# Kernel tuning notes

Hardware: AMD Instinct MI355X
Metric: run time of the kernel (lower is better)

Reference implementation:

```python
import jax, jax.numpy as jnp
import numpy as np

TIME_LEN = 8
JOINT_NUM = 22
SEQ = TIME_LEN * JOINT_NUM  # 176
H_NUM = 8
H_DIM = 64
NEG = -9e15


def build_t_mask():
    # ones everywhere, zero the 22x22 diagonal (same-frame) blocks, then add identity
    t = np.ones((SEQ, SEQ), dtype=np.float32)
    for i in range(TIME_LEN):
        b = i * JOINT_NUM
        t[b:b + JOINT_NUM, b:b + JOINT_NUM] = 0.0
    t += np.eye(SEQ, dtype=np.float32)
    return jnp.asarray(t)


def setup_inputs() -> dict:
    key = jax.random.key(0)
    ks = jax.random.split(key, 7)
    B, S, D_IN = 512, SEQ, 128
    D_MODEL = H_NUM * H_DIM
    s = 1.0 / np.sqrt(D_IN)
    return {
        "x": jax.random.normal(ks[0], (B, S, D_IN), dtype=jnp.float32),
        "Wq": jax.random.normal(ks[1], (D_IN, D_MODEL), dtype=jnp.float32) * s,
        "bq": jax.random.normal(ks[2], (D_MODEL,), dtype=jnp.float32) * 0.01,
        "Wk": jax.random.normal(ks[3], (D_IN, D_MODEL), dtype=jnp.float32) * s,
        "bk": jax.random.normal(ks[4], (D_MODEL,), dtype=jnp.float32) * 0.01,
        "Wv": jax.random.normal(ks[5], (D_IN, D_MODEL), dtype=jnp.float32) * s,
        "bv": jax.random.normal(ks[6], (D_MODEL,), dtype=jnp.float32) * 0.01,
    }


def reference(x, Wq, bq, Wk, bk, Wv, bv):
    B = x.shape[0]
    mask = build_t_mask()  # [S, S], values in {0, 1}
    # projections; dropout is inference-mode identity; value path has ReLU
    q = (x @ Wq + bq).reshape(B, -1, H_NUM, H_DIM).transpose(0, 2, 1, 3)  # [B,H,S,D]
    k = (x @ Wk + bk).reshape(B, -1, H_NUM, H_DIM).transpose(0, 2, 1, 3)
    v = jax.nn.relu(x @ Wv + bv).reshape(B, -1, H_NUM, H_DIM).transpose(0, 2, 1, 3)
    scores = jnp.einsum("bhqd,bhkd->bhqk", q, k) / jnp.sqrt(jnp.float32(H_DIM))
    # temporal domain: multiplicative mask + large-negative additive fill
    scores = scores * mask + (1.0 - mask) * NEG
    p = jax.nn.softmax(scores, axis=-1)
    out = jnp.einsum("bhqk,bhkd->bhqd", p, v)
    return out.transpose(0, 2, 1, 3).reshape(B, -1, H_NUM * H_DIM)
```

## Files before the change

kernel.cpp:

```cpp
#include <hip/hip_runtime.h>
#include <hip/hip_bf16.h>

#define JOINTS   22
#define SEQ      176
#define DIN      128
#define NHEAD    8
#define HD       64
#define DMODEL   512
#define NMT      11

typedef __bf16 bf16x8 __attribute__((ext_vector_type(8)));
typedef float  f32x4  __attribute__((ext_vector_type(4)));

__device__ __forceinline__ unsigned short f2bf(float f) {
  __hip_bfloat16 h = __float2bfloat16(f);
  return __builtin_bit_cast(unsigned short, h);
}
__device__ __forceinline__ float bf2f(unsigned short u) {
  __hip_bfloat16 h = __builtin_bit_cast(__hip_bfloat16, u);
  return __bfloat162float(h);
}

#define WT_E    0u
#define BIAS_E  196608u
#define Q_E     198144u
#define PERQKV  46137344u
#define K_E     (Q_E + PERQKV)
#define V_E     (K_E + PERQKV)
#define WS_NEED ((size_t)(V_E + PERQKV) * 2)

__global__ __launch_bounds__(256) void prep_kernel(
    const float* __restrict__ Wq, const float* __restrict__ bq,
    const float* __restrict__ Wk, const float* __restrict__ bk,
    const float* __restrict__ Wv, const float* __restrict__ bv,
    unsigned short* __restrict__ ws)
{
  int idx = blockIdx.x * 256 + threadIdx.x;
  int which = idx >> 16;
  int rem = idx & 65535;
  int n = rem >> 7, k = rem & 127;
  const float* W = (which == 0) ? Wq : (which == 1 ? Wk : Wv);
  float scale = (which == 0) ? 0.125f : 1.0f;
  ws[WT_E + idx] = f2bf(W[k * DMODEL + n] * scale);
  if (idx < 1536) {
    int w2 = idx >> 9, n2 = idx & 511;
    const float* bb = (w2 == 0) ? bq : (w2 == 1 ? bk : bv);
    float s2 = (w2 == 0) ? 0.125f : 1.0f;
    ws[BIAS_E + idx] = f2bf(bb[n2] * s2);
  }
}

__global__ __launch_bounds__(256) void qkv_gemm_kernel(
    const float* __restrict__ x, unsigned short* __restrict__ ws)
{
  __shared__ unsigned short Xs[128 * 136];
  __shared__ unsigned short Wt[128 * 136];
  const int tid  = threadIdx.x;
  const int lane = tid & 63, wave = tid >> 6;
  const int l15  = lane & 15, quad = lane >> 4;
  const int m0 = blockIdx.x * 128;
  const int nb = blockIdx.y;
  const int wm = (wave >> 1) * 64, wn = (wave & 1) * 64;

  {
    const float4* x4 = reinterpret_cast<const float4*>(x + (size_t)m0 * DIN);
    #pragma unroll
    for (int i = 0; i < 16; ++i) {
      int c = tid + i * 256;
      int row = c >> 5, col4 = c & 31;
      float4 v = x4[c];
      uint2 pk;
      pk.x = (unsigned)f2bf(v.x) | ((unsigned)f2bf(v.y) << 16);
      pk.y = (unsigned)f2bf(v.z) | ((unsigned)f2bf(v.w) << 16);
      *reinterpret_cast<uint2*>(&Xs[row * 136 + col4 * 4]) = pk;
    }
  }

  for (int which = 0; which < 3; ++which) {
    __syncthreads();
    {
      const uint4* wsrc = reinterpret_cast<const uint4*>(
          ws + WT_E + which * 65536 + nb * 128 * 128);
      #pragma unroll
      for (int i = 0; i < 8; ++i) {
        int c = tid + i * 256;
        int row = c >> 4, col8 = c & 15;
        *reinterpret_cast<uint4*>(&Wt[row * 136 + col8 * 8]) = wsrc[c];
      }
    }
    __syncthreads();

    f32x4 acc[16];
    #pragma unroll
    for (int i = 0; i < 16; ++i) acc[i] = (f32x4){0.f, 0.f, 0.f, 0.f};

    #pragma unroll
    for (int kk = 0; kk < 4; ++kk) {
      bf16x8 a[4], bfr[4];
      #pragma unroll
      for (int mt = 0; mt < 4; ++mt)
        a[mt] = *reinterpret_cast<const bf16x8*>(
            &Xs[(wm + mt * 16 + l15) * 136 + kk * 32 + quad * 8]);
      #pragma unroll
      for (int nt = 0; nt < 4; ++nt)
        bfr[nt] = *reinterpret_cast<const bf16x8*>(
            &Wt[(wn + nt * 16 + l15) * 136 + kk * 32 + quad * 8]);
      if (which != 2) {
        #pragma unroll
        for (int mt = 0; mt < 4; ++mt)
          #pragma unroll
          for (int nt = 0; nt < 4; ++nt)
            acc[mt * 4 + nt] = __builtin_amdgcn_mfma_f32_16x16x32_bf16(
                a[mt], bfr[nt], acc[mt * 4 + nt], 0, 0, 0);
      } else {
        #pragma unroll
        for (int mt = 0; mt < 4; ++mt)
          #pragma unroll
          for (int nt = 0; nt < 4; ++nt)
            acc[mt * 4 + nt] = __builtin_amdgcn_mfma_f32_16x16x32_bf16(
                bfr[nt], a[mt], acc[mt * 4 + nt], 0, 0, 0);
      }
    }

    if (which != 2) {
      unsigned short* dst = ws + ((which == 0) ? Q_E : K_E);
      #pragma unroll
      for (int nt = 0; nt < 4; ++nt) {
        int c = nb * 128 + wn + nt * 16 + l15;
        float bs = bf2f(ws[BIAS_E + which * 512 + c]);
        int h = c >> 6, d = c & 63;
        #pragma unroll
        for (int mt = 0; mt < 4; ++mt) {
          #pragma unroll
          for (int r = 0; r < 4; ++r) {
            int g = m0 + wm + mt * 16 + quad * 4 + r;
            int b_ = g / 176, s = g - b_ * 176;
            dst[((size_t)(b_ * 8 + h) * 176 + s) * 64 + d] =
                f2bf(acc[mt * 4 + nt][r] + bs);
          }
        }
      }
    } else {
      unsigned short* dst = ws + V_E;
      #pragma unroll
      for (int nt = 0; nt < 4; ++nt) {
        #pragma unroll
        for (int r = 0; r < 4; ++r) {
          int c = nb * 128 + wn + nt * 16 + quad * 4 + r;
          int h = c >> 6, d = c & 63;
          float bs = bf2f(ws[BIAS_E + 1024 + c]);
          #pragma unroll
          for (int mt = 0; mt < 4; ++mt) {
            int g = m0 + wm + mt * 16 + l15;
            int b_ = g / 176, s = g - b_ * 176;
            float val = fmaxf(acc[mt * 4 + nt][r] + bs, 0.f);
            dst[((size_t)(b_ * 8 + h) * 64 + d) * 176 + s] = f2bf(val);
          }
        }
      }
    }
  }
}

#define KLD 72
#define VLD 184
#define PLD 184

__global__ __launch_bounds__(256) void attn_kernel(
    const unsigned short* __restrict__ ws, float* __restrict__ out)
{
  __shared__ unsigned short Ks[SEQ * KLD];
  __shared__ unsigned short Vt[HD * VLD];
  __shared__ unsigned short Ps[4][16 * PLD];

  const int tid  = threadIdx.x;
  const int lane = tid & 63, wave = tid >> 6;
  const int l15  = lane & 15, quad = lane >> 4;
  const int bh = blockIdx.x;
  const int b = bh >> 3, h = bh & 7;

  const unsigned short* qp = ws + Q_E + (size_t)bh * 11264;
  const unsigned short* kp = ws + K_E + (size_t)bh * 11264;
  const unsigned short* vp = ws + V_E + (size_t)bh * 11264;

  const uint4 z4 = {0u, 0u, 0u, 0u};
  const bf16x8 zfrag = __builtin_bit_cast(bf16x8, z4);

  bf16x8 aq[3][2];
  #pragma unroll
  for (int i = 0; i < 3; ++i) {
    int mt = wave + 4 * i;
    if (mt < NMT) {
      aq[i][0] = *reinterpret_cast<const bf16x8*>(qp + (mt * 16 + l15) * 64 + quad * 8);
      aq[i][1] = *reinterpret_cast<const bf16x8*>(qp + (mt * 16 + l15) * 64 + 32 + quad * 8);
    }
  }

  {
    const uint4* ks4 = reinterpret_cast<const uint4*>(kp);
    #pragma unroll
    for (int i = 0; i < 6; ++i) {
      int c = tid + i * 256;
      if (c < 1408) {
        int row = c >> 3, col = c & 7;
        *reinterpret_cast<uint4*>(&Ks[row * KLD + col * 8]) = ks4[c];
      }
    }
  }
  {
    const uint4* vs4 = reinterpret_cast<const uint4*>(vp);
    #pragma unroll
    for (int i = 0; i < 6; ++i) {
      int c = tid + i * 256;
      if (c < 1408) {
        int row = c / 22, col = c - row * 22;
        *reinterpret_cast<uint4*>(&Vt[row * VLD + col * 8]) = vs4[c];
      }
    }
  }
  __syncthreads();

  unsigned short* Pw = Ps[wave];

  int cdiv[NMT];
  #pragma unroll
  for (int nt = 0; nt < NMT; ++nt) cdiv[nt] = (nt * 16 + l15) / JOINTS;

  #pragma unroll
  for (int i = 0; i < 3; ++i) {
    int mt = wave + 4 * i;
    if (mt < NMT) {
      f32x4 sc[NMT];
      #pragma unroll
      for (int nt = 0; nt < NMT; ++nt) {
        bf16x8 k0 = *reinterpret_cast<const bf16x8*>(
            &Ks[(nt * 16 + l15) * KLD + quad * 8]);
        bf16x8 k1 = *reinterpret_cast<const bf16x8*>(
            &Ks[(nt * 16 + l15) * KLD + 32 + quad * 8]);
        f32x4 acc = {0.f, 0.f, 0.f, 0.f};
        acc = __builtin_amdgcn_mfma_f32_16x16x32_bf16(aq[i][0], k0, acc, 0, 0, 0);
        acc = __builtin_amdgcn_mfma_f32_16x16x32_bf16(aq[i][1], k1, acc, 0, 0, 0);
        sc[nt] = acc;
      }

      float rinv[4];
      #pragma unroll
      for (int r = 0; r < 4; ++r) {
        const int q  = mt * 16 + quad * 4 + r;
        const int fq = q / JOINTS;
        float mx = -3.0e38f;
        #pragma unroll
        for (int nt = 0; nt < NMT; ++nt) {
          int c = nt * 16 + l15;
          bool masked = (cdiv[nt] == fq) && (c != q);
          float v = masked ? -1.0e30f : sc[nt][r];
          sc[nt][r] = v;
          mx = fmaxf(mx, v);
        }
        mx = fmaxf(mx, __shfl_xor(mx, 1));
        mx = fmaxf(mx, __shfl_xor(mx, 2));
        mx = fmaxf(mx, __shfl_xor(mx, 4));
        mx = fmaxf(mx, __shfl_xor(mx, 8));
        float sum = 0.f;
        #pragma unroll
        for (int nt = 0; nt < NMT; ++nt) {
          float e = __expf(sc[nt][r] - mx);
          sc[nt][r] = e;
          sum += e;
        }
        sum += __shfl_xor(sum, 1);
        sum += __shfl_xor(sum, 2);
        sum += __shfl_xor(sum, 4);
        sum += __shfl_xor(sum, 8);
        rinv[r] = 1.0f / sum;
      }

      #pragma unroll
      for (int nt = 0; nt < NMT; ++nt)
        #pragma unroll
        for (int r = 0; r < 4; ++r)
          Pw[(quad * 4 + r) * PLD + nt * 16 + l15] = f2bf(sc[nt][r]);

      #pragma unroll
      for (int nt_o = 0; nt_o < 4; ++nt_o) {
        f32x4 acc = {0.f, 0.f, 0.f, 0.f};
        #pragma unroll
        for (int kk = 0; kk < 6; ++kk) {
          bool act = (kk < 5) || (quad < 2);
          int off = act ? (kk * 32 + quad * 8) : 0;
          bf16x8 ap = *reinterpret_cast<const bf16x8*>(&Pw[l15 * PLD + off]);
          bf16x8 bv = *reinterpret_cast<const bf16x8*>(
              &Vt[(nt_o * 16 + l15) * VLD + off]);
          if (!act) { ap = zfrag; bv = zfrag; }
          acc = __builtin_amdgcn_mfma_f32_16x16x32_bf16(ap, bv, acc, 0, 0, 0);
        }
        #pragma unroll
        for (int r = 0; r < 4; ++r) {
          int q = mt * 16 + quad * 4 + r;
          out[((size_t)b * SEQ + q) * DMODEL + h * HD + nt_o * 16 + l15] =
              acc[r] * rinv[r];
        }
      }
    }
  }
}

#define BLK      704
#define XS_LD 136
#define WS_LD 136
#define QK_LD 72
#define PV_LD 184

struct __align__(16) SMem {
  union {
    struct {
      unsigned short Xs[SEQ * XS_LD];
      unsigned short Ws[HD  * WS_LD];
    } p1;
    unsigned short Ps[SEQ * PV_LD];
  } u;
  unsigned short Qs[SEQ * QK_LD];
  unsigned short Ks[SEQ * QK_LD];
  unsigned short Vt[HD  * PV_LD];
};

__global__ __launch_bounds__(BLK) void mha_fused_kernel(
    const float* __restrict__ x,
    const float* __restrict__ Wq, const float* __restrict__ bq,
    const float* __restrict__ Wk, const float* __restrict__ bk,
    const float* __restrict__ Wv, const float* __restrict__ bv,
    float* __restrict__ out)
{
  __shared__ SMem sm;
  const int tid  = threadIdx.x;
  const int lane = tid & 63;
  const int wave = tid >> 6;
  const int l15  = lane & 15;
  const int quad = lane >> 4;
  const int b    = blockIdx.x >> 3;
  const int h    = blockIdx.x & 7;

  const uint4 z4 = {0u, 0u, 0u, 0u};
  const bf16x8 zfrag = __builtin_bit_cast(bf16x8, z4);

  {
    const float4* xg = reinterpret_cast<const float4*>(x + (size_t)b * (SEQ * DIN));
    #pragma unroll
    for (int i = 0; i < 8; ++i) {
      int c = tid + i * BLK;
      int row  = c >> 5;
      int col4 = c & 31;
      float4 v = xg[c];
      uint2 pk;
      pk.x = (unsigned)f2bf(v.x) | ((unsigned)f2bf(v.y) << 16);
      pk.y = (unsigned)f2bf(v.z) | ((unsigned)f2bf(v.w) << 16);
      *reinterpret_cast<uint2*>(&sm.u.p1.Xs[row * XS_LD + col4 * 4]) = pk;
    }
  }

  const float* Wptr[3] = {Wq, Wk, Wv};
  const float* Bptr[3] = {bq, bk, bv};

  for (int m = 0; m < 3; ++m) {
    for (int k = wave; k < DIN; k += NMT)
      sm.u.p1.Ws[lane * WS_LD + k] = f2bf(Wptr[m][(size_t)k * DMODEL + h * HD + lane]);
    __syncthreads();

    const int mt = wave;
    bf16x8 a[4];
    #pragma unroll
    for (int kk = 0; kk < 4; ++kk)
      a[kk] = *reinterpret_cast<const bf16x8*>(
          &sm.u.p1.Xs[(mt * 16 + l15) * XS_LD + kk * 32 + quad * 8]);

    #pragma unroll
    for (int nt = 0; nt < 4; ++nt) {
      f32x4 acc = {0.f, 0.f, 0.f, 0.f};
      #pragma unroll
      for (int kk = 0; kk < 4; ++kk) {
        bf16x8 bb = *reinterpret_cast<const bf16x8*>(
            &sm.u.p1.Ws[(nt * 16 + l15) * WS_LD + kk * 32 + quad * 8]);
        acc = __builtin_amdgcn_mfma_f32_16x16x32_bf16(a[kk], bb, acc, 0, 0, 0);
      }
      float bs = Bptr[m][h * HD + nt * 16 + l15];
      if (m == 0) {
        #pragma unroll
        for (int r = 0; r < 4; ++r)
          sm.Qs[(mt * 16 + quad * 4 + r) * QK_LD + nt * 16 + l15] =
              f2bf((acc[r] + bs) * 0.125f);
      } else if (m == 1) {
        #pragma unroll
        for (int r = 0; r < 4; ++r)
          sm.Ks[(mt * 16 + quad * 4 + r) * QK_LD + nt * 16 + l15] =
              f2bf(acc[r] + bs);
      } else {
        float v0 = fmaxf(acc[0] + bs, 0.f), v1 = fmaxf(acc[1] + bs, 0.f);
        float v2 = fmaxf(acc[2] + bs, 0.f), v3 = fmaxf(acc[3] + bs, 0.f);
        uint2 pk;
        pk.x = (unsigned)f2bf(v0) | ((unsigned)f2bf(v1) << 16);
        pk.y = (unsigned)f2bf(v2) | ((unsigned)f2bf(v3) << 16);
        *reinterpret_cast<uint2*>(
            &sm.Vt[(nt * 16 + l15) * PV_LD + mt * 16 + quad * 4]) = pk;
      }
    }
    __syncthreads();
  }

  {
    const int mt = wave;
    bf16x8 aq0 = *reinterpret_cast<const bf16x8*>(
        &sm.Qs[(mt * 16 + l15) * QK_LD + 0 + quad * 8]);
    bf16x8 aq1 = *reinterpret_cast<const bf16x8*>(
        &sm.Qs[(mt * 16 + l15) * QK_LD + 32 + quad * 8]);

    f32x4 sc[NMT];
    #pragma unroll
    for (int nt = 0; nt < NMT; ++nt) {
      f32x4 acc = {0.f, 0.f, 0.f, 0.f};
      bf16x8 k0 = *reinterpret_cast<const bf16x8*>(
          &sm.Ks[(nt * 16 + l15) * QK_LD + 0 + quad * 8]);
      bf16x8 k1 = *reinterpret_cast<const bf16x8*>(
          &sm.Ks[(nt * 16 + l15) * QK_LD + 32 + quad * 8]);
      acc = __builtin_amdgcn_mfma_f32_16x16x32_bf16(aq0, k0, acc, 0, 0, 0);
      acc = __builtin_amdgcn_mfma_f32_16x16x32_bf16(aq1, k1, acc, 0, 0, 0);
      sc[nt] = acc;
    }

    float rinv[4];
    #pragma unroll
    for (int r = 0; r < 4; ++r) {
      const int q  = mt * 16 + quad * 4 + r;
      const int fq = q / JOINTS;
      float mx = -3.0e38f;
      #pragma unroll
      for (int nt = 0; nt < NMT; ++nt) {
        int c = nt * 16 + l15;
        bool masked = ((c / JOINTS) == fq) && (c != q);
        float v = masked ? -1.0e30f : sc[nt][r];
        sc[nt][r] = v;
        mx = fmaxf(mx, v);
      }
      mx = fmaxf(mx, __shfl_xor(mx, 1));
      mx = fmaxf(mx, __shfl_xor(mx, 2));
      mx = fmaxf(mx, __shfl_xor(mx, 4));
      mx = fmaxf(mx, __shfl_xor(mx, 8));
      float sum = 0.f;
      #pragma unroll
      for (int nt = 0; nt < NMT; ++nt) {
        float e = __expf(sc[nt][r] - mx);
        sum += e;
        sm.u.Ps[q * PV_LD + nt * 16 + l15] = f2bf(e);
      }
      sum += __shfl_xor(sum, 1);
      sum += __shfl_xor(sum, 2);
      sum += __shfl_xor(sum, 4);
      sum += __shfl_xor(sum, 8);
      rinv[r] = 1.0f / sum;
    }

    #pragma unroll
    for (int nt = 0; nt < 4; ++nt) {
      f32x4 acc = {0.f, 0.f, 0.f, 0.f};
      #pragma unroll
      for (int kk = 0; kk < 6; ++kk) {
        bool act = (kk < 5) || (quad < 2);
        int off = act ? (kk * 32 + quad * 8) : 0;
        bf16x8 ap  = *reinterpret_cast<const bf16x8*>(
            &sm.u.Ps[(mt * 16 + l15) * PV_LD + off]);
        bf16x8 bv8 = *reinterpret_cast<const bf16x8*>(
            &sm.Vt[(nt * 16 + l15) * PV_LD + off]);
        if (!act) { ap = zfrag; bv8 = zfrag; }
        acc = __builtin_amdgcn_mfma_f32_16x16x32_bf16(ap, bv8, acc, 0, 0, 0);
      }
      #pragma unroll
      for (int r = 0; r < 4; ++r) {
        int q = mt * 16 + quad * 4 + r;
        out[((size_t)b * SEQ + q) * DMODEL + h * HD + nt * 16 + l15] =
            acc[r] * rinv[r];
      }
    }
  }
}

extern "C" void kernel_launch(void* const* d_in, const int* in_sizes, int n_in,
                              void* d_out, int out_size, void* d_ws, size_t ws_size,
                              hipStream_t stream) {
  const float* x  = (const float*)d_in[0];
  const float* Wq = (const float*)d_in[1];
  const float* bq = (const float*)d_in[2];
  const float* Wk = (const float*)d_in[3];
  const float* bk = (const float*)d_in[4];
  const float* Wv = (const float*)d_in[5];
  const float* bv = (const float*)d_in[6];
  const int B = in_sizes[0] / (SEQ * DIN);

  if (ws_size >= WS_NEED && B == 512) {
    unsigned short* ws = (unsigned short*)d_ws;
    hipLaunchKernelGGL(prep_kernel, dim3(768), dim3(256), 0, stream,
                       Wq, bq, Wk, bk, Wv, bv, ws);
    hipLaunchKernelGGL(qkv_gemm_kernel, dim3(704, 4), dim3(256), 0, stream,
                       x, ws);
    hipLaunchKernelGGL(attn_kernel, dim3(4096), dim3(256), 0, stream,
                       (const unsigned short*)ws, (float*)d_out);
  } else {
    hipLaunchKernelGGL(mha_fused_kernel, dim3(B * NHEAD), dim3(BLK), 0, stream,
                       x, Wq, bq, Wk, bk, Wv, bv, (float*)d_out);
  }
}
```

Before: 487.8 us.

## Transpose QK^T MFMA so each lane owns a query row, vectorize P stores

Swaps the MFMA operands so the score tile is transposed: each lane holds one query row across four key columns. Softmax reductions then need only two cross-quad shuffles instead of four per row, and the mask becomes a simple range test. Normalization moves before the bf16 P store, which is now packed into 8-byte writes, and P fragments are hoisted out of the PV loop. The mt<NMT guard is dropped from the compute path, so the last wave does redundant work and reads past the Q tile, with only the output store guarded.

```diff
diff --git a/kernel.cpp b/kernel.cpp
--- a/kernel.cpp
+++ b/kernel.cpp
@@ -190,10 +190,8 @@
   #pragma unroll
   for (int i = 0; i < 3; ++i) {
     int mt = wave + 4 * i;
-    if (mt < NMT) {
-      aq[i][0] = *reinterpret_cast<const bf16x8*>(qp + (mt * 16 + l15) * 64 + quad * 8);
-      aq[i][1] = *reinterpret_cast<const bf16x8*>(qp + (mt * 16 + l15) * 64 + 32 + quad * 8);
-    }
+    aq[i][0] = *reinterpret_cast<const bf16x8*>(qp + (mt * 16 + l15) * 64 + quad * 8);
+    aq[i][1] = *reinterpret_cast<const bf16x8*>(qp + (mt * 16 + l15) * 64 + 32 + quad * 8);
   }
 
   {
@@ -222,83 +220,97 @@
 
   unsigned short* Pw = Ps[wave];
 
-  int cdiv[NMT];
-  #pragma unroll
-  for (int nt = 0; nt < NMT; ++nt) cdiv[nt] = (nt * 16 + l15) / JOINTS;
-
   #pragma unroll
   for (int i = 0; i < 3; ++i) {
-    int mt = wave + 4 * i;
-    if (mt < NMT) {
-      f32x4 sc[NMT];
-      #pragma unroll
-      for (int nt = 0; nt < NMT; ++nt) {
-        bf16x8 k0 = *reinterpret_cast<const bf16x8*>(
-            &Ks[(nt * 16 + l15) * KLD + quad * 8]);
-        bf16x8 k1 = *reinterpret_cast<const bf16x8*>(
-            &Ks[(nt * 16 + l15) * KLD + 32 + quad * 8]);
-        f32x4 acc = {0.f, 0.f, 0.f, 0.f};
-        acc = __builtin_amdgcn_mfma_f32_16x16x32_bf16(aq[i][0], k0, acc, 0, 0, 0);
-        acc = __builtin_amdgcn_mfma_f32_16x16x32_bf16(aq[i][1], k1, acc, 0, 0, 0);
-        sc[nt] = acc;
-      }
-
-      float rinv[4];
+    const int mt = wave + 4 * i;
+
+    f32x4 sc[NMT];
+    #pragma unroll
+    for (int nt = 0; nt < NMT; ++nt) {
+      bf16x8 k0 = *reinterpret_cast<const bf16x8*>(
+          &Ks[(nt * 16 + l15) * KLD + quad * 8]);
+      bf16x8 k1 = *reinterpret_cast<const bf16x8*>(
+          &Ks[(nt * 16 + l15) * KLD + 32 + quad * 8]);
+      f32x4 acc = {0.f, 0.f, 0.f, 0.f};
+      acc = __builtin_amdgcn_mfma_f32_16x16x32_bf16(k0, aq[i][0], acc, 0, 0, 0);
+      acc = __builtin_amdgcn_mfma_f32_16x16x32_bf16(k1, aq[i][1], acc, 0, 0, 0);
+      sc[nt] = acc;
+    }
+
+    const int q  = mt * 16 + l15;
+    const int lo = (q / JOINTS) * JOINTS;
+    const int hi = lo + JOINTS;
+
+    float mx0 = -3.0e38f, mx1 = -3.0e38f, mx2 = -3.0e38f, mx3 = -3.0e38f;
+    #pragma unroll
+    for (int nt = 0; nt < NMT; ++nt) {
       #pragma unroll
       for (int r = 0; r < 4; ++r) {
-        const int q  = mt * 16 + quad * 4 + r;
-        const int fq = q / JOINTS;
-        float mx = -3.0e38f;
-        #pragma unroll
-        for (int nt = 0; nt < NMT; ++nt) {
-          int c = nt * 16 + l15;
-          bool masked = (cdiv[nt] == fq) && (c != q);
-          float v = masked ? -1.0e30f : sc[nt][r];
-          sc[nt][r] = v;
-          mx = fmaxf(mx, v);
-        }
-        mx = fmaxf(mx, __shfl_xor(mx, 1));
-        mx = fmaxf(mx, __shfl_xor(mx, 2));
-        mx = fmaxf(mx, __shfl_xor(mx, 4));
-        mx = fmaxf(mx, __shfl_xor(mx, 8));
-        float sum = 0.f;
-        #pragma unroll
-        for (int nt = 0; nt < NMT; ++nt) {
-          float e = __expf(sc[nt][r] - mx);
-          sc[nt][r] = e;
-          sum += e;
-        }
-        sum += __shfl_xor(sum, 1);
-        sum += __shfl_xor(sum, 2);
-        sum += __shfl_xor(sum, 4);
-        sum += __shfl_xor(sum, 8);
-        rinv[r] = 1.0f / sum;
-      }
-
-      #pragma unroll
-      for (int nt = 0; nt < NMT; ++nt)
-        #pragma unroll
-        for (int r = 0; r < 4; ++r)
-          Pw[(quad * 4 + r) * PLD + nt * 16 + l15] = f2bf(sc[nt][r]);
-
-      #pragma unroll
-      for (int nt_o = 0; nt_o < 4; ++nt_o) {
-        f32x4 acc = {0.f, 0.f, 0.f, 0.f};
-        #pragma unroll
-        for (int kk = 0; kk < 6; ++kk) {
-          bool act = (kk < 5) || (quad < 2);
-          int off = act ? (kk * 32 + quad * 8) : 0;
-          bf16x8 ap = *reinterpret_cast<const bf16x8*>(&Pw[l15 * PLD + off]);
-          bf16x8 bv = *reinterpret_cast<const bf16x8*>(
-              &Vt[(nt_o * 16 + l15) * VLD + off]);
-          if (!act) { ap = zfrag; bv = zfrag; }
-          acc = __builtin_amdgcn_mfma_f32_16x16x32_bf16(ap, bv, acc, 0, 0, 0);
-        }
+        int k = nt * 16 + quad * 4 + r;
+        bool msk = (k >= lo) && (k < hi) && (k != q);
+        float v = msk ? -1.0e30f : sc[nt][r];
+        sc[nt][r] = v;
+        if (r == 0) mx0 = fmaxf(mx0, v);
+        else if (r == 1) mx1 = fmaxf(mx1, v);
+        else if (r == 2) mx2 = fmaxf(mx2, v);
+        else mx3 = fmaxf(mx3, v);
+      }
+    }
+    float mx = fmaxf(fmaxf(mx0, mx1), fmaxf(mx2, mx3));
+    mx = fmaxf(mx, __shfl_xor(mx, 16));
+    mx = fmaxf(mx, __shfl_xor(mx, 32));
+
+    float s0 = 0.f, s1 = 0.f, s2 = 0.f, s3 = 0.f;
+    #pragma unroll
+    for (int nt = 0; nt < NMT; ++nt) {
+      float e0 = __expf(sc[nt][0] - mx);
+      float e1 = __expf(sc[nt][1] - mx);
+      float e2 = __expf(sc[nt][2] - mx);
+      float e3 = __expf(sc[nt][3] - mx);
+      sc[nt][0] = e0; sc[nt][1] = e1; sc[nt][2] = e2; sc[nt][3] = e3;
+      s0 += e0; s1 += e1; s2 += e2; s3 += e3;
+    }
+    float sum = (s0 + s1) + (s2 + s3);
+    sum += __shfl_xor(sum, 16);
+    sum += __shfl_xor(sum, 32);
+    float rinv = 1.0f / sum;
+
+    #pragma unroll
+    for (int nt = 0; nt < NMT; ++nt) {
+      float p0 = sc[nt][0] * rinv, p1 = sc[nt][1] * rinv;
+      float p2 = sc[nt][2] * rinv, p3 = sc[nt][3] * rinv;
+      uint2 pk;
+      pk.x = (unsigned)f2bf(p0) | ((unsigned)f2bf(p1) << 16);
+      pk.y = (unsigned)f2bf(p2) | ((unsigned)f2bf(p3) << 16);
+      *reinterpret_cast<uint2*>(&Pw[l15 * PLD + nt * 16 + quad * 4]) = pk;
+    }
+
+    bf16x8 ap[6];
+    #pragma unroll
+    for (int kk = 0; kk < 6; ++kk) {
+      bool act = (kk < 5) || (quad < 2);
+      int off = act ? (kk * 32 + quad * 8) : 0;
+      bf16x8 v = *reinterpret_cast<const bf16x8*>(&Pw[l15 * PLD + off]);
+      ap[kk] = act ? v : zfrag;
+    }
+
+    #pragma unroll
+    for (int nt_o = 0; nt_o < 4; ++nt_o) {
+      f32x4 acc = {0.f, 0.f, 0.f, 0.f};
+      #pragma unroll
+      for (int kk = 0; kk < 6; ++kk) {
+        bool act = (kk < 5) || (quad < 2);
+        int off = act ? (kk * 32 + quad * 8) : 0;
+        bf16x8 bv = *reinterpret_cast<const bf16x8*>(
+            &Vt[(nt_o * 16 + l15) * VLD + off]);
+        acc = __builtin_amdgcn_mfma_f32_16x16x32_bf16(ap[kk], bv, acc, 0, 0, 0);
+      }
+      if (mt < NMT) {
         #pragma unroll
         for (int r = 0; r < 4; ++r) {
-          int q = mt * 16 + quad * 4 + r;
-          out[((size_t)b * SEQ + q) * DMODEL + h * HD + nt_o * 16 + l15] =
-              acc[r] * rinv[r];
+          int qq = mt * 16 + quad * 4 + r;
+          out[((size_t)b * SEQ + qq) * DMODEL + h * HD + nt_o * 16 + l15] =
+              acc[r];
         }
       }
     }
```

Measured after the change: 471.1 us. 1.04x faster.

## Rewrite attention kernel with 32x32 MFMA and register-resident probabilities

Applied to the files above, without the earlier changes.

Recasts the attention kernel onto 32x32x16 MFMA tiles, computing S^T so that each lane holds a full query column of scores. The softmax then needs only one cross-lane shuffle, and the normalized probabilities feed the PV MFMA straight from registers instead of going through a per-wave LDS staging buffer. Blocks grow to 6 waves (384 threads) with K and V padded to 192 keys, which adds wasted padded work and raises register pressure.

```diff
diff --git a/kernel.cpp b/kernel.cpp
--- a/kernel.cpp
+++ b/kernel.cpp
@@ -11,6 +11,7 @@
 
 typedef __bf16 bf16x8 __attribute__((ext_vector_type(8)));
 typedef float  f32x4  __attribute__((ext_vector_type(4)));
+typedef float  f32x16 __attribute__((ext_vector_type(16)));
 
 __device__ __forceinline__ unsigned short f2bf(float f) {
   __hip_bfloat16 h = __float2bfloat16(f);
@@ -162,20 +163,18 @@
   }
 }
 
-#define KLD 72
-#define VLD 184
-#define PLD 184
-
-__global__ __launch_bounds__(256) void attn_kernel(
+#define KLD32 66
+#define VLD32 194
+
+__global__ __launch_bounds__(384, 3) void attn_kernel(
     const unsigned short* __restrict__ ws, float* __restrict__ out)
 {
-  __shared__ unsigned short Ks[SEQ * KLD];
-  __shared__ unsigned short Vt[HD * VLD];
-  __shared__ unsigned short Ps[4][16 * PLD];
+  __shared__ unsigned short Ks[192 * KLD32];
+  __shared__ unsigned short Vt[HD * VLD32];
 
   const int tid  = threadIdx.x;
   const int lane = tid & 63, wave = tid >> 6;
-  const int l15  = lane & 15, quad = lane >> 4;
+  const int l31  = lane & 31, hi = lane >> 5;
   const int bh = blockIdx.x;
   const int b = bh >> 3, h = bh & 7;
 
@@ -183,124 +182,145 @@
   const unsigned short* kp = ws + K_E + (size_t)bh * 11264;
   const unsigned short* vp = ws + V_E + (size_t)bh * 11264;
 
-  const uint4 z4 = {0u, 0u, 0u, 0u};
-  const bf16x8 zfrag = __builtin_bit_cast(bf16x8, z4);
-
-  bf16x8 aq[3][2];
-  #pragma unroll
-  for (int i = 0; i < 3; ++i) {
-    int mt = wave + 4 * i;
-    if (mt < NMT) {
-      aq[i][0] = *reinterpret_cast<const bf16x8*>(qp + (mt * 16 + l15) * 64 + quad * 8);
-      aq[i][1] = *reinterpret_cast<const bf16x8*>(qp + (mt * 16 + l15) * 64 + 32 + quad * 8);
-    }
-  }
+  const int q = wave * 32 + l31;
+  bf16x8 aq[4];
+  #pragma unroll
+  for (int dt = 0; dt < 4; ++dt)
+    aq[dt] = *reinterpret_cast<const bf16x8*>(qp + q * 64 + dt * 16 + hi * 8);
 
   {
     const uint4* ks4 = reinterpret_cast<const uint4*>(kp);
-    #pragma unroll
-    for (int i = 0; i < 6; ++i) {
-      int c = tid + i * 256;
-      if (c < 1408) {
-        int row = c >> 3, col = c & 7;
-        *reinterpret_cast<uint4*>(&Ks[row * KLD + col * 8]) = ks4[c];
-      }
+    const uint4 z = {0u, 0u, 0u, 0u};
+    #pragma unroll
+    for (int i = 0; i < 4; ++i) {
+      int c = tid + i * 384;
+      int row = c >> 3, col = c & 7;
+      uint4 v = (c < 1408) ? ks4[c] : z;
+      *reinterpret_cast<uint4*>(&Ks[row * KLD32 + col * 8]) = v;
     }
   }
   {
     const uint4* vs4 = reinterpret_cast<const uint4*>(vp);
-    #pragma unroll
-    for (int i = 0; i < 6; ++i) {
-      int c = tid + i * 256;
+    const uint4 z = {0u, 0u, 0u, 0u};
+    #pragma unroll
+    for (int i = 0; i < 4; ++i) {
+      int c = tid + i * 384;
       if (c < 1408) {
         int row = c / 22, col = c - row * 22;
-        *reinterpret_cast<uint4*>(&Vt[row * VLD + col * 8]) = vs4[c];
+        *reinterpret_cast<uint4*>(&Vt[row * VLD32 + col * 8]) = vs4[c];
+      } else {
+        int c2 = c - 1408;
+        int row = c2 >> 1, col = c2 & 1;
+        *reinterpret_cast<uint4*>(&Vt[row * VLD32 + 176 + col * 8]) = z;
       }
     }
   }
   __syncthreads();
 
-  unsigned short* Pw = Ps[wave];
-
-  int cdiv[NMT];
-  #pragma unroll
-  for (int nt = 0; nt < NMT; ++nt) cdiv[nt] = (nt * 16 + l15) / JOINTS;
-
-  #pragma unroll
-  for (int i = 0; i < 3; ++i) {
-    int mt = wave + 4 * i;
-    if (mt < NMT) {
-      f32x4 sc[NMT];
-      #pragma unroll
-      for (int nt = 0; nt < NMT; ++nt) {
-        bf16x8 k0 = *reinterpret_cast<const bf16x8*>(
-            &Ks[(nt * 16 + l15) * KLD + quad * 8]);
-        bf16x8 k1 = *reinterpret_cast<const bf16x8*>(
-            &Ks[(nt * 16 + l15) * KLD + 32 + quad * 8]);
-        f32x4 acc = {0.f, 0.f, 0.f, 0.f};
-        acc = __builtin_amdgcn_mfma_f32_16x16x32_bf16(aq[i][0], k0, acc, 0, 0, 0);
-        acc = __builtin_amdgcn_mfma_f32_16x16x32_bf16(aq[i][1], k1, acc, 0, 0, 0);
-        sc[nt] = acc;
-      }
-
-      float rinv[4];
-      #pragma unroll
-      for (int r = 0; r < 4; ++r) {
-        const int q  = mt * 16 + quad * 4 + r;
-        const int fq = q / JOINTS;
-        float mx = -3.0e38f;
-        #pragma unroll
-        for (int nt = 0; nt < NMT; ++nt) {
-          int c = nt * 16 + l15;
-          bool masked = (cdiv[nt] == fq) && (c != q);
-          float v = masked ? -1.0e30f : sc[nt][r];
-          sc[nt][r] = v;
-          mx = fmaxf(mx, v);
-        }
-        mx = fmaxf(mx, __shfl_xor(mx, 1));
-        mx = fmaxf(mx, __shfl_xor(mx, 2));
-        mx = fmaxf(mx, __shfl_xor(mx, 4));
-        mx = fmaxf(mx, __shfl_xor(mx, 8));
-        float sum = 0.f;
-        #pragma unroll
-        for (int nt = 0; nt < NMT; ++nt) {
-          float e = __expf(sc[nt][r] - mx);
-          sc[nt][r] = e;
-          sum += e;
-        }
-        sum += __shfl_xor(sum, 1);
-        sum += __shfl_xor(sum, 2);
-        sum += __shfl_xor(sum, 4);
-        sum += __shfl_xor(sum, 8);
-        rinv[r] = 1.0f / sum;
-      }
-
-      #pragma unroll
-      for (int nt = 0; nt < NMT; ++nt)
-        #pragma unroll
-        for (int r = 0; r < 4; ++r)
-          Pw[(quad * 4 + r) * PLD + nt * 16 + l15] = f2bf(sc[nt][r]);
-
-      #pragma unroll
-      for (int nt_o = 0; nt_o < 4; ++nt_o) {
-        f32x4 acc = {0.f, 0.f, 0.f, 0.f};
-        #pragma unroll
-        for (int kk = 0; kk < 6; ++kk) {
-          bool act = (kk < 5) || (quad < 2);
-          int off = act ? (kk * 32 + quad * 8) : 0;
-          bf16x8 ap = *reinterpret_cast<const bf16x8*>(&Pw[l15 * PLD + off]);
-          bf16x8 bv = *reinterpret_cast<const bf16x8*>(
-              &Vt[(nt_o * 16 + l15) * VLD + off]);
-          if (!act) { ap = zfrag; bv = zfrag; }
-          acc = __builtin_amdgcn_mfma_f32_16x16x32_bf16(ap, bv, acc, 0, 0, 0);
-        }
-        #pragma unroll
-        for (int r = 0; r < 4; ++r) {
-          int q = mt * 16 + quad * 4 + r;
-          out[((size_t)b * SEQ + q) * DMODEL + h * HD + nt_o * 16 + l15] =
-              acc[r] * rinv[r];
-        }
-      }
+  f32x16 sc[6];
+  #pragma unroll
+  for (int nt = 0; nt < 6; ++nt) {
+    f32x16 acc;
+    #pragma unroll
+    for (int zz = 0; zz < 16; ++zz) acc[zz] = 0.f;
+    #pragma unroll
+    for (int dt = 0; dt < 4; ++dt) {
+      bf16x8 kf = *reinterpret_cast<const bf16x8*>(
+          &Ks[(nt * 32 + l31) * KLD32 + dt * 16 + hi * 8]);
+      acc = __builtin_amdgcn_mfma_f32_32x32x16_bf16(kf, aq[dt], acc, 0, 0, 0);
+    }
+    sc[nt] = acc;
+  }
+
+  const int lo   = (q / JOINTS) * JOINTS;
+  const int hifr = lo + JOINTS;
+  float mxa0 = -3.0e38f, mxa1 = -3.0e38f, mxa2 = -3.0e38f, mxa3 = -3.0e38f;
+  #pragma unroll
+  for (int nt = 0; nt < 6; ++nt) {
+    #pragma unroll
+    for (int reg = 0; reg < 16; ++reg) {
+      int k = nt * 32 + (reg & 3) + 8 * (reg >> 2) + 4 * hi;
+      bool msk = (k >= SEQ) || ((k >= lo) && (k < hifr) && (k != q));
+      float v = msk ? -1.0e30f : sc[nt][reg];
+      sc[nt][reg] = v;
+      if ((reg & 3) == 0) mxa0 = fmaxf(mxa0, v);
+      else if ((reg & 3) == 1) mxa1 = fmaxf(mxa1, v);
+      else if ((reg & 3) == 2) mxa2 = fmaxf(mxa2, v);
+      else mxa3 = fmaxf(mxa3, v);
+    }
+  }
+  float mx = fmaxf(fmaxf(mxa0, mxa1), fmaxf(mxa2, mxa3));
+  mx = fmaxf(mx, __shfl_xor(mx, 32));
+
+  float sa0 = 0.f, sa1 = 0.f, sa2 = 0.f, sa3 = 0.f;
+  #pragma unroll
+  for (int nt = 0; nt < 6; ++nt) {
+    #pragma unroll
+    for (int reg = 0; reg < 16; ++reg) {
+      float e = __expf(sc[nt][reg] - mx);
+      sc[nt][reg] = e;
+      if ((reg & 3) == 0) sa0 += e;
+      else if ((reg & 3) == 1) sa1 += e;
+      else if ((reg & 3) == 2) sa2 += e;
+      else sa3 += e;
+    }
+  }
+  float sum = (sa0 + sa1) + (sa2 + sa3);
+  sum += __shfl_xor(sum, 32);
+  float rinv = 1.0f / sum;
+
+  uint4 pa[6][2];
+  #pragma unroll
+  for (int nt = 0; nt < 6; ++nt) {
+    #pragma unroll
+    for (int hf = 0; hf < 2; ++hf) {
+      unsigned w0, w1, w2, w3;
+      {
+        float a0 = sc[nt][hf * 8 + 0] * rinv, a1 = sc[nt][hf * 8 + 1] * rinv;
+        float a2 = sc[nt][hf * 8 + 2] * rinv, a3 = sc[nt][hf * 8 + 3] * rinv;
+        float a4 = sc[nt][hf * 8 + 4] * rinv, a5 = sc[nt][hf * 8 + 5] * rinv;
+        float a6 = sc[nt][hf * 8 + 6] * rinv, a7 = sc[nt][hf * 8 + 7] * rinv;
+        w0 = (unsigned)f2bf(a0) | ((unsigned)f2bf(a1) << 16);
+        w1 = (unsigned)f2bf(a2) | ((unsigned)f2bf(a3) << 16);
+        w2 = (unsigned)f2bf(a4) | ((unsigned)f2bf(a5) << 16);
+        w3 = (unsigned)f2bf(a6) | ((unsigned)f2bf(a7) << 16);
+      }
+      pa[nt][hf].x = w0; pa[nt][hf].y = w1; pa[nt][hf].z = w2; pa[nt][hf].w = w3;
+    }
+  }
+
+  f32x16 ov[2];
+  #pragma unroll
+  for (int dt = 0; dt < 2; ++dt) {
+    #pragma unroll
+    for (int zz = 0; zz < 16; ++zz) ov[dt][zz] = 0.f;
+  }
+  #pragma unroll
+  for (int nt = 0; nt < 6; ++nt) {
+    #pragma unroll
+    for (int hf = 0; hf < 2; ++hf) {
+      bf16x8 af = __builtin_bit_cast(bf16x8, pa[nt][hf]);
+      const int base = nt * 32 + 16 * hf + 4 * hi;
+      #pragma unroll
+      for (int dt = 0; dt < 2; ++dt) {
+        const unsigned short* vrow = &Vt[(dt * 32 + l31) * VLD32];
+        uint2 blo = *reinterpret_cast<const uint2*>(vrow + base);
+        uint2 bhi = *reinterpret_cast<const uint2*>(vrow + base + 8);
+        uint4 bb4; bb4.x = blo.x; bb4.y = blo.y; bb4.z = bhi.x; bb4.w = bhi.y;
+        bf16x8 bf = __builtin_bit_cast(bf16x8, bb4);
+        ov[dt] = __builtin_amdgcn_mfma_f32_32x32x16_bf16(af, bf, ov[dt], 0, 0, 0);
+      }
+    }
+  }
+
+  #pragma unroll
+  for (int dt = 0; dt < 2; ++dt) {
+    int d = dt * 32 + l31;
+    #pragma unroll
+    for (int reg = 0; reg < 16; ++reg) {
+      int qq = wave * 32 + (reg & 3) + 8 * (reg >> 2) + 4 * hi;
+      if (qq < SEQ)
+        out[((size_t)b * SEQ + qq) * DMODEL + h * HD + d] = ov[dt][reg];
     }
   }
 }
@@ -500,7 +520,7 @@
                        Wq, bq, Wk, bk, Wv, bv, ws);
     hipLaunchKernelGGL(qkv_gemm_kernel, dim3(704, 4), dim3(256), 0, stream,
                        x, ws);
-    hipLaunchKernelGGL(attn_kernel, dim3(4096), dim3(256), 0, stream,
+    hipLaunchKernelGGL(attn_kernel, dim3(4096), dim3(384), 0, stream,
                        (const unsigned short*)ws, (float*)d_out);
   } else {
     hipLaunchKernelGGL(mha_fused_kernel, dim3(B * NHEAD), dim3(BLK), 0, stream,
```

After: 590.7 us. +21.1%, slower.
